# Kernel tuning notes

Hardware: AMD Instinct MI355X
Metric: run time of the kernel (lower is better)

The kernel has to match this reference:

```python
import jax, jax.numpy as jnp
import numpy as np


def setup_inputs() -> dict:
    key = jax.random.key(0)
    k1, k2 = jax.random.split(key)
    B, Lq, Lv, D = 16, 2048, 2048, 1024
    query = jax.random.normal(k1, (B, Lq, D), dtype=jnp.float32)
    value = jax.random.normal(k2, (B, Lv, D), dtype=jnp.float32)
    return {"query": query, "value": value}


def reference(query, value):
    # score[b,q,k] = sum_d query[b,q,d] * value[b,k,d]   (NO 1/sqrt(d) scaling,
    # matching the original torch module)
    score = jnp.einsum("bqd,bkd->bqk", query, value)
    attn = jax.nn.softmax(score, axis=-1)  # softmax over the value/key axis
    context = jnp.einsum("bqk,bkd->bqd", attn, value)
    return (context, attn)
```

## Files before the change

kernel.cpp:

```cpp
#include <hip/hip_runtime.h>

typedef __bf16 bf16_t;
typedef __attribute__((ext_vector_type(4))) __bf16 bf16x4;
typedef __attribute__((ext_vector_type(8))) __bf16 bf16x8;
typedef __attribute__((ext_vector_type(4))) float f32x4;

constexpr int BATCH = 16;
constexpr int LQ = 2048;
constexpr int LV = 2048;
constexpr int DIM = 1024;

constexpr int BM = 128, BN = 128, BK = 32;

typedef __attribute__((address_space(1))) const unsigned int g_u32;
typedef __attribute__((address_space(3))) unsigned int l_u32;
__device__ __forceinline__ void glds16(const void* g, void* l) {
    __builtin_amdgcn_global_load_lds((g_u32*)g, (l_u32*)l, 16, 0, 0);
}

__global__ __launch_bounds__(256)
void prep_kernel(const float4* __restrict__ src, bf16x4* __restrict__ hi,
                 bf16x4* __restrict__ lo, int n4) {
    int i = blockIdx.x * 256 + threadIdx.x;
    const int stride = gridDim.x * 256;
    for (; i < n4; i += stride) {
        const float4 x = src[i];
        const float xs[4] = {x.x, x.y, x.z, x.w};
        bf16x4 h, l;
#pragma unroll
        for (int e = 0; e < 4; ++e) {
            bf16_t hh = (bf16_t)xs[e];
            h[e] = hh;
            l[e] = (bf16_t)(xs[e] - (float)hh);
        }
        hi[i] = h;
        lo[i] = l;
    }
}

__global__ __launch_bounds__(256)
void vt_kernel(const float* __restrict__ V, bf16_t* __restrict__ VT) {
    __shared__ float tile[64][33];
    const int b  = blockIdx.z;
    const int k0 = blockIdx.x * 64;
    const int d0 = blockIdx.y * 32;
    const int tid = threadIdx.x;
    const float* Vb  = V  + (size_t)b * LV * DIM;
    bf16_t*      VTb = VT + (size_t)b * DIM * LV;

    const int r = tid >> 3;
    const int c = (tid & 7) * 4;
#pragma unroll
    for (int h = 0; h < 2; ++h) {
        const float4 x = *(const float4*)(Vb + (size_t)(k0 + r + h * 32) * DIM + d0 + c);
        tile[r + h * 32][c]     = x.x;
        tile[r + h * 32][c + 1] = x.y;
        tile[r + h * 32][c + 2] = x.z;
        tile[r + h * 32][c + 3] = x.w;
    }
    __syncthreads();
    const int dd = tid >> 3;
    const int kk = (tid & 7) * 8;
    bf16x8 o;
#pragma unroll
    for (int j = 0; j < 8; ++j) o[j] = (bf16_t)tile[kk + j][dd];
    *(bf16x8*)&VTb[(size_t)(d0 + dd) * LV + k0 + kk] = o;
}

__global__ __launch_bounds__(256, 3)
void gemm1_glds(const bf16_t* __restrict__ Qh, const bf16_t* __restrict__ Ql,
                const bf16_t* __restrict__ Vh, const bf16_t* __restrict__ Vl,
                float* __restrict__ S) {
    __shared__ __align__(16) bf16_t Ah[BM][BK];
    __shared__ __align__(16) bf16_t Al[BM][BK];
    __shared__ __align__(16) bf16_t Bh[BN][BK];
    __shared__ __align__(16) bf16_t Bl[BN][BK];

    const int b  = blockIdx.z;
    const int m0 = blockIdx.y * BM;
    const int n0 = blockIdx.x * BN;
    const bf16_t* Qhb = Qh + (size_t)b * LQ * DIM;
    const bf16_t* Qlb = Ql + (size_t)b * LQ * DIM;
    const bf16_t* Vhb = Vh + (size_t)b * LV * DIM;
    const bf16_t* Vlb = Vl + (size_t)b * LV * DIM;
    float*        Sb  = S  + (size_t)b * LQ * LV;

    const int tid  = threadIdx.x;
    const int lane = tid & 63;
    const int wave = tid >> 6;
    const int wm   = (wave >> 1) * 64;
    const int wn   = (wave & 1) * 64;
    const int l15  = lane & 15;
    const int quad = lane >> 4;

    const int srow = tid >> 2;
    const int sseg = (tid & 3) * 8;

    f32x4 acc[4][4];
#pragma unroll
    for (int i = 0; i < 4; ++i)
#pragma unroll
        for (int j = 0; j < 4; ++j) {
            f32x4 z = {0.f, 0.f, 0.f, 0.f};
            acc[i][j] = z;
        }

    for (int k0 = 0; k0 < DIM; k0 += BK) {
        glds16(Qhb + (size_t)(m0 + srow) * DIM + k0 + sseg,      &Ah[srow][sseg]);
        glds16(Qhb + (size_t)(m0 + srow + 64) * DIM + k0 + sseg, &Ah[srow + 64][sseg]);
        glds16(Qlb + (size_t)(m0 + srow) * DIM + k0 + sseg,      &Al[srow][sseg]);
        glds16(Qlb + (size_t)(m0 + srow + 64) * DIM + k0 + sseg, &Al[srow + 64][sseg]);
        glds16(Vhb + (size_t)(n0 + srow) * DIM + k0 + sseg,      &Bh[srow][sseg]);
        glds16(Vhb + (size_t)(n0 + srow + 64) * DIM + k0 + sseg, &Bh[srow + 64][sseg]);
        glds16(Vlb + (size_t)(n0 + srow) * DIM + k0 + sseg,      &Bl[srow][sseg]);
        glds16(Vlb + (size_t)(n0 + srow + 64) * DIM + k0 + sseg, &Bl[srow + 64][sseg]);
        __syncthreads();

        bf16x8 ah[4], al[4], bh[4], bl[4];
#pragma unroll
        for (int i = 0; i < 4; ++i) {
            ah[i] = *(const bf16x8*)&Ah[wm + i * 16 + l15][quad * 8];
            al[i] = *(const bf16x8*)&Al[wm + i * 16 + l15][quad * 8];
            bh[i] = *(const bf16x8*)&Bh[wn + i * 16 + l15][quad * 8];
            bl[i] = *(const bf16x8*)&Bl[wn + i * 16 + l15][quad * 8];
        }
#pragma unroll
        for (int i = 0; i < 4; ++i)
#pragma unroll
            for (int j = 0; j < 4; ++j) {
                acc[i][j] = __builtin_amdgcn_mfma_f32_16x16x32_bf16(ah[i], bh[j], acc[i][j], 0, 0, 0);
                acc[i][j] = __builtin_amdgcn_mfma_f32_16x16x32_bf16(ah[i], bl[j], acc[i][j], 0, 0, 0);
                acc[i][j] = __builtin_amdgcn_mfma_f32_16x16x32_bf16(al[i], bh[j], acc[i][j], 0, 0, 0);
            }
        __syncthreads();
    }

#pragma unroll
    for (int i = 0; i < 4; ++i)
#pragma unroll
        for (int j = 0; j < 4; ++j)
#pragma unroll
            for (int r = 0; r < 4; ++r) {
                const int row = m0 + wm + i * 16 + quad * 4 + r;
                const int col = n0 + wn + j * 16 + l15;
                Sb[(size_t)row * LV + col] = acc[i][j][r];
            }
}

__global__ __launch_bounds__(256)
void softmax_b16(float* __restrict__ S, bf16_t* __restrict__ S16) {
    __shared__ float red[8];
    const size_t row = blockIdx.x;
    float* p = S + row * (size_t)LV;
    bf16_t* p16 = S16 + row * (size_t)LV;
    const int tid  = threadIdx.x;
    const int lane = tid & 63;
    const int wave = tid >> 6;

    float4 v0 = ((const float4*)p)[tid];
    float4 v1 = ((const float4*)p)[tid + 256];

    float m = fmaxf(fmaxf(fmaxf(v0.x, v0.y), fmaxf(v0.z, v0.w)),
                    fmaxf(fmaxf(v1.x, v1.y), fmaxf(v1.z, v1.w)));
#pragma unroll
    for (int off = 32; off > 0; off >>= 1) m = fmaxf(m, __shfl_xor(m, off));
    if (lane == 0) red[wave] = m;
    __syncthreads();
    m = fmaxf(fmaxf(red[0], red[1]), fmaxf(red[2], red[3]));

    float e0 = __expf(v0.x - m), e1 = __expf(v0.y - m);
    float e2 = __expf(v0.z - m), e3 = __expf(v0.w - m);
    float e4 = __expf(v1.x - m), e5 = __expf(v1.y - m);
    float e6 = __expf(v1.z - m), e7 = __expf(v1.w - m);

    float s = ((e0 + e1) + (e2 + e3)) + ((e4 + e5) + (e6 + e7));
#pragma unroll
    for (int off = 32; off > 0; off >>= 1) s += __shfl_xor(s, off);
    if (lane == 0) red[4 + wave] = s;
    __syncthreads();
    s = (red[4] + red[5]) + (red[6] + red[7]);

    const float inv = 1.0f / s;
    v0.x = e0 * inv; v0.y = e1 * inv; v0.z = e2 * inv; v0.w = e3 * inv;
    v1.x = e4 * inv; v1.y = e5 * inv; v1.z = e6 * inv; v1.w = e7 * inv;
    ((float4*)p)[tid]       = v0;
    ((float4*)p)[tid + 256] = v1;

    bf16x4 h0, h1;
    h0[0] = (bf16_t)v0.x; h0[1] = (bf16_t)v0.y; h0[2] = (bf16_t)v0.z; h0[3] = (bf16_t)v0.w;
    h1[0] = (bf16_t)v1.x; h1[1] = (bf16_t)v1.y; h1[2] = (bf16_t)v1.z; h1[3] = (bf16_t)v1.w;
    ((bf16x4*)p16)[tid]       = h0;
    ((bf16x4*)p16)[tid + 256] = h1;
}

__global__ __launch_bounds__(256, 3)
void gemm2_glds(const bf16_t* __restrict__ P16, const bf16_t* __restrict__ VT,
                float* __restrict__ C) {
    __shared__ __align__(16) bf16_t As[BM][BK];
    __shared__ __align__(16) bf16_t Bs[BN][BK];

    const int b  = blockIdx.z;
    const int m0 = blockIdx.y * BM;
    const int n0 = blockIdx.x * BN;
    const bf16_t* Pb = P16 + (size_t)b * LQ * LV;
    const bf16_t* Vb = VT  + (size_t)b * DIM * LV;
    float*        Cb = C   + (size_t)b * LQ * DIM;

    const int tid  = threadIdx.x;
    const int lane = tid & 63;
    const int wave = tid >> 6;
    const int wm   = (wave >> 1) * 64;
    const int wn   = (wave & 1) * 64;
    const int l15  = lane & 15;
    const int quad = lane >> 4;

    const int srow = tid >> 2;
    const int sseg = (tid & 3) * 8;

    f32x4 acc[4][4];
#pragma unroll
    for (int i = 0; i < 4; ++i)
#pragma unroll
        for (int j = 0; j < 4; ++j) {
            f32x4 z = {0.f, 0.f, 0.f, 0.f};
            acc[i][j] = z;
        }

    for (int k0 = 0; k0 < LV; k0 += BK) {
        glds16(Pb + (size_t)(m0 + srow) * LV + k0 + sseg,      &As[srow][sseg]);
        glds16(Pb + (size_t)(m0 + srow + 64) * LV + k0 + sseg, &As[srow + 64][sseg]);
        glds16(Vb + (size_t)(n0 + srow) * LV + k0 + sseg,      &Bs[srow][sseg]);
        glds16(Vb + (size_t)(n0 + srow + 64) * LV + k0 + sseg, &Bs[srow + 64][sseg]);
        __syncthreads();

        bf16x8 af[4], bfr[4];
#pragma unroll
        for (int i = 0; i < 4; ++i) {
            af[i]  = *(const bf16x8*)&As[wm + i * 16 + l15][quad * 8];
            bfr[i] = *(const bf16x8*)&Bs[wn + i * 16 + l15][quad * 8];
        }
#pragma unroll
        for (int i = 0; i < 4; ++i)
#pragma unroll
            for (int j = 0; j < 4; ++j)
                acc[i][j] = __builtin_amdgcn_mfma_f32_16x16x32_bf16(af[i], bfr[j], acc[i][j], 0, 0, 0);
        __syncthreads();
    }

#pragma unroll
    for (int i = 0; i < 4; ++i)
#pragma unroll
        for (int j = 0; j < 4; ++j)
#pragma unroll
            for (int r = 0; r < 4; ++r) {
                const int row = m0 + wm + i * 16 + quad * 4 + r;
                const int col = n0 + wn + j * 16 + l15;
                Cb[(size_t)row * DIM + col] = acc[i][j][r];
            }
}

__global__ __launch_bounds__(256, 2)
void gemm1_fb(const float* __restrict__ Q, const float* __restrict__ V,
              float* __restrict__ S) {
    __shared__ __align__(16) bf16_t Ahi[BM][BK];
    __shared__ __align__(16) bf16_t Alo[BM][BK];
    __shared__ __align__(16) bf16_t Bhi[BN][BK];
    __shared__ __align__(16) bf16_t Blo[BN][BK];

    const int b  = blockIdx.z;
    const int m0 = blockIdx.y * BM;
    const int n0 = blockIdx.x * BN;
    const float* Qb = Q + (size_t)b * LQ * DIM;
    const float* Vb = V + (size_t)b * LV * DIM;
    float*       Sb = S + (size_t)b * LQ * LV;

    const int tid  = threadIdx.x;
    const int lane = tid & 63;
    const int wave = tid >> 6;
    const int wm   = (wave >> 1) * 64;
    const int wn   = (wave & 1) * 64;
    const int l15  = lane & 15;
    const int quad = lane >> 4;
    const int srow = tid >> 3;
    const int scol = (tid & 7) * 4;

    f32x4 acc[4][4];
#pragma unroll
    for (int i = 0; i < 4; ++i)
#pragma unroll
        for (int j = 0; j < 4; ++j) {
            f32x4 z = {0.f, 0.f, 0.f, 0.f};
            acc[i][j] = z;
        }

    for (int k0 = 0; k0 < DIM; k0 += BK) {
#pragma unroll
        for (int p = 0; p < 4; ++p) {
            const int r = p * 32 + srow;
            const float4 qa = *(const float4*)(Qb + (size_t)(m0 + r) * DIM + k0 + scol);
            const float4 va = *(const float4*)(Vb + (size_t)(n0 + r) * DIM + k0 + scol);
            const float qx[4] = {qa.x, qa.y, qa.z, qa.w};
            const float vx[4] = {va.x, va.y, va.z, va.w};
            bf16x4 qh, ql, vh, vl;
#pragma unroll
            for (int e = 0; e < 4; ++e) {
                bf16_t h = (bf16_t)qx[e];
                qh[e] = h; ql[e] = (bf16_t)(qx[e] - (float)h);
                bf16_t h2 = (bf16_t)vx[e];
                vh[e] = h2; vl[e] = (bf16_t)(vx[e] - (float)h2);
            }
            *(bf16x4*)&Ahi[r][scol] = qh;
            *(bf16x4*)&Alo[r][scol] = ql;
            *(bf16x4*)&Bhi[r][scol] = vh;
            *(bf16x4*)&Blo[r][scol] = vl;
        }
        __syncthreads();
        bf16x8 ah[4], al[4], bh[4], bl[4];
#pragma unroll
        for (int i = 0; i < 4; ++i) {
            ah[i] = *(const bf16x8*)&Ahi[wm + i * 16 + l15][quad * 8];
            al[i] = *(const bf16x8*)&Alo[wm + i * 16 + l15][quad * 8];
            bh[i] = *(const bf16x8*)&Bhi[wn + i * 16 + l15][quad * 8];
            bl[i] = *(const bf16x8*)&Blo[wn + i * 16 + l15][quad * 8];
        }
#pragma unroll
        for (int i = 0; i < 4; ++i)
#pragma unroll
            for (int j = 0; j < 4; ++j) {
                acc[i][j] = __builtin_amdgcn_mfma_f32_16x16x32_bf16(ah[i], bh[j], acc[i][j], 0, 0, 0);
                acc[i][j] = __builtin_amdgcn_mfma_f32_16x16x32_bf16(ah[i], bl[j], acc[i][j], 0, 0, 0);
                acc[i][j] = __builtin_amdgcn_mfma_f32_16x16x32_bf16(al[i], bh[j], acc[i][j], 0, 0, 0);
            }
        __syncthreads();
    }
#pragma unroll
    for (int i = 0; i < 4; ++i)
#pragma unroll
        for (int j = 0; j < 4; ++j)
#pragma unroll
            for (int r = 0; r < 4; ++r) {
                const int row = m0 + wm + i * 16 + quad * 4 + r;
                const int col = n0 + wn + j * 16 + l15;
                Sb[(size_t)row * LV + col] = acc[i][j][r];
            }
}

__global__ __launch_bounds__(256)
void softmax_fb(float* __restrict__ S) {
    __shared__ float red[8];
    const size_t row = blockIdx.x;
    float* p = S + row * (size_t)LV;
    const int tid  = threadIdx.x;
    const int lane = tid & 63;
    const int wave = tid >> 6;
    float4 v0 = ((const float4*)p)[tid];
    float4 v1 = ((const float4*)p)[tid + 256];
    float m = fmaxf(fmaxf(fmaxf(v0.x, v0.y), fmaxf(v0.z, v0.w)),
                    fmaxf(fmaxf(v1.x, v1.y), fmaxf(v1.z, v1.w)));
#pragma unroll
    for (int off = 32; off > 0; off >>= 1) m = fmaxf(m, __shfl_xor(m, off));
    if (lane == 0) red[wave] = m;
    __syncthreads();
    m = fmaxf(fmaxf(red[0], red[1]), fmaxf(red[2], red[3]));
    float e0 = __expf(v0.x - m), e1 = __expf(v0.y - m);
    float e2 = __expf(v0.z - m), e3 = __expf(v0.w - m);
    float e4 = __expf(v1.x - m), e5 = __expf(v1.y - m);
    float e6 = __expf(v1.z - m), e7 = __expf(v1.w - m);
    float s = ((e0 + e1) + (e2 + e3)) + ((e4 + e5) + (e6 + e7));
#pragma unroll
    for (int off = 32; off > 0; off >>= 1) s += __shfl_xor(s, off);
    if (lane == 0) red[4 + wave] = s;
    __syncthreads();
    s = (red[4] + red[5]) + (red[6] + red[7]);
    const float inv = 1.0f / s;
    v0.x = e0 * inv; v0.y = e1 * inv; v0.z = e2 * inv; v0.w = e3 * inv;
    v1.x = e4 * inv; v1.y = e5 * inv; v1.z = e6 * inv; v1.w = e7 * inv;
    ((float4*)p)[tid]       = v0;
    ((float4*)p)[tid + 256] = v1;
}

__global__ __launch_bounds__(256, 2)
void gemm2_fb(const float* __restrict__ P, const bf16_t* __restrict__ VT,
              float* __restrict__ C) {
    __shared__ __align__(16) bf16_t As[BM][BK];
    __shared__ __align__(16) bf16_t Bs[BN][BK];
    const int b  = blockIdx.z;
    const int m0 = blockIdx.y * BM;
    const int n0 = blockIdx.x * BN;
    const float*  Pb = P  + (size_t)b * LQ * LV;
    const bf16_t* Vb = VT + (size_t)b * DIM * LV;
    float*        Cb = C  + (size_t)b * LQ * DIM;
    const int tid  = threadIdx.x;
    const int lane = tid & 63;
    const int wave = tid >> 6;
    const int wm   = (wave >> 1) * 64;
    const int wn   = (wave & 1) * 64;
    const int l15  = lane & 15;
    const int quad = lane >> 4;
    const int arow = tid >> 3;
    const int acol = (tid & 7) * 4;
    const int brow = tid >> 2;
    const int bseg = (tid & 3) * 8;
    f32x4 acc[4][4];
#pragma unroll
    for (int i = 0; i < 4; ++i)
#pragma unroll
        for (int j = 0; j < 4; ++j) {
            f32x4 z = {0.f, 0.f, 0.f, 0.f};
            acc[i][j] = z;
        }
    for (int k0 = 0; k0 < LV; k0 += BK) {
#pragma unroll
        for (int p4 = 0; p4 < 4; ++p4) {
            const int r = p4 * 32 + arow;
            const float4 a = *(const float4*)(Pb + (size_t)(m0 + r) * LV + k0 + acol);
            bf16x4 hv;
            hv[0] = (bf16_t)a.x; hv[1] = (bf16_t)a.y;
            hv[2] = (bf16_t)a.z; hv[3] = (bf16_t)a.w;
            *(bf16x4*)&As[r][acol] = hv;
        }
#pragma unroll
        for (int p4 = 0; p4 < 2; ++p4) {
            const int r = p4 * 64 + brow;
            *(bf16x8*)&Bs[r][bseg] =
                *(const bf16x8*)(Vb + (size_t)(n0 + r) * LV + k0 + bseg);
        }
        __syncthreads();
        bf16x8 af[4], bfr[4];
#pragma unroll
        for (int i = 0; i < 4; ++i) {
            af[i]  = *(const bf16x8*)&As[wm + i * 16 + l15][quad * 8];
            bfr[i] = *(const bf16x8*)&Bs[wn + i * 16 + l15][quad * 8];
        }
#pragma unroll
        for (int i = 0; i < 4; ++i)
#pragma unroll
            for (int j = 0; j < 4; ++j)
                acc[i][j] = __builtin_amdgcn_mfma_f32_16x16x32_bf16(af[i], bfr[j], acc[i][j], 0, 0, 0);
        __syncthreads();
    }
#pragma unroll
    for (int i = 0; i < 4; ++i)
#pragma unroll
        for (int j = 0; j < 4; ++j)
#pragma unroll
            for (int r = 0; r < 4; ++r) {
                const int row = m0 + wm + i * 16 + quad * 4 + r;
                const int col = n0 + wn + j * 16 + l15;
                Cb[(size_t)row * DIM + col] = acc[i][j][r];
            }
}

extern "C" void kernel_launch(void* const* d_in, const int* in_sizes, int n_in,
                              void* d_out, int out_size, void* d_ws, size_t ws_size,
                              hipStream_t stream) {
    const float* Q = (const float*)d_in[0];
    const float* V = (const float*)d_in[1];
    float* ctx  = (float*)d_out;
    float* attn = ctx + (size_t)BATCH * LQ * DIM;
    char* ws = (char*)d_ws;

    const size_t EL = (size_t)BATCH * LQ * DIM;
    const size_t SZ = EL * sizeof(bf16_t);

    if (ws_size >= 5 * SZ) {
        bf16_t* Qh  = (bf16_t*)ws;
        bf16_t* Ql  = Qh + EL;
        bf16_t* Vh  = Ql + EL;
        bf16_t* Vl  = Vh + EL;
        bf16_t* VT  = (bf16_t*)(ws + 4 * SZ);
        bf16_t* P16 = (bf16_t*)ws;

        prep_kernel<<<4096, 256, 0, stream>>>((const float4*)Q, (bf16x4*)Qh, (bf16x4*)Ql, (int)(EL / 4));
        prep_kernel<<<4096, 256, 0, stream>>>((const float4*)V, (bf16x4*)Vh, (bf16x4*)Vl, (int)(EL / 4));
        vt_kernel<<<dim3(LV / 64, DIM / 32, BATCH), 256, 0, stream>>>(V, VT);
        gemm1_glds<<<dim3(LV / BN, LQ / BM, BATCH), 256, 0, stream>>>(Qh, Ql, Vh, Vl, attn);
        softmax_b16<<<BATCH * LQ, 256, 0, stream>>>(attn, P16);
        gemm2_glds<<<dim3(DIM / BN, LQ / BM, BATCH), 256, 0, stream>>>(P16, VT, ctx);
    } else if (ws_size >= 3 * SZ) {
        bf16_t* VT  = (bf16_t*)ws;
        bf16_t* P16 = (bf16_t*)(ws + SZ);
        vt_kernel<<<dim3(LV / 64, DIM / 32, BATCH), 256, 0, stream>>>(V, VT);
        gemm1_fb<<<dim3(LV / BN, LQ / BM, BATCH), 256, 0, stream>>>(Q, V, attn);
        softmax_b16<<<BATCH * LQ, 256, 0, stream>>>(attn, P16);
        gemm2_glds<<<dim3(DIM / BN, LQ / BM, BATCH), 256, 0, stream>>>(P16, VT, ctx);
    } else {
        bf16_t* VT = (bf16_t*)ws;
        vt_kernel<<<dim3(LV / 64, DIM / 32, BATCH), 256, 0, stream>>>(V, VT);
        gemm1_fb<<<dim3(LV / BN, LQ / BM, BATCH), 256, 0, stream>>>(Q, V, attn);
        softmax_fb<<<BATCH * LQ, 256, 0, stream>>>(attn);
        gemm2_fb<<<dim3(DIM / BN, LQ / BM, BATCH), 256, 0, stream>>>(attn, VT, ctx);
    }
}
```

Before: 1.264 ms.

## Rewrite score GEMM with 256x256 tiles, double-buffered LDS and swizzle

Replaces the first GEMM (split bf16 hi/lo, three MFMAs per product) with a 512-thread kernel that computes 256x256 output tiles. It double-buffers K-slices in 128KB of dynamic LDS via global_load_lds, swizzles the LDS layout to avoid bank conflicts, and interleaves fragment loads with MFMA quadrants under s_setprio. The aim is more data reuse per loaded byte and overlap of global loads with compute. In exchange it uses much more LDS and more registers per thread, which lowers occupancy, and relies on manual vmcnt waits and many barriers.

```diff
diff --git a/kernel.cpp b/kernel.cpp
--- a/kernel.cpp
+++ b/kernel.cpp
@@ -67,18 +67,16 @@
     *(bf16x8*)&VTb[(size_t)(d0 + dd) * LV + k0 + kk] = o;
 }
 
-__global__ __launch_bounds__(256, 3)
-void gemm1_glds(const bf16_t* __restrict__ Qh, const bf16_t* __restrict__ Ql,
-                const bf16_t* __restrict__ Vh, const bf16_t* __restrict__ Vl,
-                float* __restrict__ S) {
-    __shared__ __align__(16) bf16_t Ah[BM][BK];
-    __shared__ __align__(16) bf16_t Al[BM][BK];
-    __shared__ __align__(16) bf16_t Bh[BN][BK];
-    __shared__ __align__(16) bf16_t Bl[BN][BK];
+__global__ __launch_bounds__(512, 2)
+void gemm1_v2(const bf16_t* __restrict__ Qh, const bf16_t* __restrict__ Ql,
+              const bf16_t* __restrict__ Vh, const bf16_t* __restrict__ Vl,
+              float* __restrict__ S) {
+    extern __shared__ __align__(16) char smem[];
+    bf16_t* lds = (bf16_t*)smem;
 
     const int b  = blockIdx.z;
-    const int m0 = blockIdx.y * BM;
-    const int n0 = blockIdx.x * BN;
+    const int m0 = blockIdx.y * 256;
+    const int n0 = blockIdx.x * 256;
     const bf16_t* Qhb = Qh + (size_t)b * LQ * DIM;
     const bf16_t* Qlb = Ql + (size_t)b * LQ * DIM;
     const bf16_t* Vhb = Vh + (size_t)b * LV * DIM;
@@ -88,55 +86,112 @@
     const int tid  = threadIdx.x;
     const int lane = tid & 63;
     const int wave = tid >> 6;
-    const int wm   = (wave >> 1) * 64;
-    const int wn   = (wave & 1) * 64;
+    const int wm   = (wave >> 2) * 128;
+    const int wn   = (wave & 3) * 64;
     const int l15  = lane & 15;
     const int quad = lane >> 4;
+    const int swz  = (l15 >> 1) & 3;
+    const int rq   = (quad ^ swz) * 8;
 
     const int srow = tid >> 2;
-    const int sseg = (tid & 3) * 8;
-
-    f32x4 acc[4][4];
-#pragma unroll
-    for (int i = 0; i < 4; ++i)
+    const int sseg = (((tid & 3) ^ ((tid >> 3) & 3)) * 8);
+    const int sdst = tid * 8;
+
+#define STAGE8(BUF, K0) do {                                                        \
+    bf16_t* Lb = lds + (BUF) * 32768;                                               \
+    glds16(Qhb + (size_t)(m0 + srow      ) * DIM + (K0) + sseg, Lb +         sdst); \
+    glds16(Qhb + (size_t)(m0 + srow + 128) * DIM + (K0) + sseg, Lb +  4096 + sdst); \
+    glds16(Qlb + (size_t)(m0 + srow      ) * DIM + (K0) + sseg, Lb +  8192 + sdst); \
+    glds16(Qlb + (size_t)(m0 + srow + 128) * DIM + (K0) + sseg, Lb + 12288 + sdst); \
+    glds16(Vhb + (size_t)(n0 + srow      ) * DIM + (K0) + sseg, Lb + 16384 + sdst); \
+    glds16(Vhb + (size_t)(n0 + srow + 128) * DIM + (K0) + sseg, Lb + 20480 + sdst); \
+    glds16(Vlb + (size_t)(n0 + srow      ) * DIM + (K0) + sseg, Lb + 24576 + sdst); \
+    glds16(Vlb + (size_t)(n0 + srow + 128) * DIM + (K0) + sseg, Lb + 28672 + sdst); \
+} while (0)
+
+#define LOADA(QI) do {                                                       \
+    _Pragma("unroll")                                                        \
+    for (int ii = 0; ii < 4; ++ii) {                                         \
+        const int row = wm + ((QI) * 4 + ii) * 16 + l15;                     \
+        ah[ii] = *(const bf16x8*)(bufp +        row * 32 + rq);              \
+        al[ii] = *(const bf16x8*)(bufp + 8192 + row * 32 + rq);              \
+    }                                                                        \
+} while (0)
+
+#define LOADB(QJ) do {                                                       \
+    _Pragma("unroll")                                                        \
+    for (int jj = 0; jj < 2; ++jj) {                                         \
+        const int row = wn + ((QJ) * 2 + jj) * 16 + l15;                     \
+        bh[(QJ) * 2 + jj] = *(const bf16x8*)(bufp + 16384 + row * 32 + rq);  \
+        bl[(QJ) * 2 + jj] = *(const bf16x8*)(bufp + 24576 + row * 32 + rq);  \
+    }                                                                        \
+} while (0)
+
+#define MFMAQ(QI, QJ) do {                                                   \
+    _Pragma("unroll")                                                        \
+    for (int ii = 0; ii < 4; ++ii)                                           \
+    _Pragma("unroll")                                                        \
+    for (int jj = 0; jj < 2; ++jj)                                           \
+        acc[(QI)*4+ii][(QJ)*2+jj] = __builtin_amdgcn_mfma_f32_16x16x32_bf16( \
+            ah[ii], bh[(QJ)*2+jj], acc[(QI)*4+ii][(QJ)*2+jj], 0, 0, 0);      \
+    _Pragma("unroll")                                                        \
+    for (int ii = 0; ii < 4; ++ii)                                           \
+    _Pragma("unroll")                                                        \
+    for (int jj = 0; jj < 2; ++jj)                                           \
+        acc[(QI)*4+ii][(QJ)*2+jj] = __builtin_amdgcn_mfma_f32_16x16x32_bf16( \
+            ah[ii], bl[(QJ)*2+jj], acc[(QI)*4+ii][(QJ)*2+jj], 0, 0, 0);      \
+    _Pragma("unroll")                                                        \
+    for (int ii = 0; ii < 4; ++ii)                                           \
+    _Pragma("unroll")                                                        \
+    for (int jj = 0; jj < 2; ++jj)                                           \
+        acc[(QI)*4+ii][(QJ)*2+jj] = __builtin_amdgcn_mfma_f32_16x16x32_bf16( \
+            al[ii], bh[(QJ)*2+jj], acc[(QI)*4+ii][(QJ)*2+jj], 0, 0, 0);      \
+} while (0)
+
+    f32x4 acc[8][4];
+#pragma unroll
+    for (int i = 0; i < 8; ++i)
 #pragma unroll
         for (int j = 0; j < 4; ++j) {
             f32x4 z = {0.f, 0.f, 0.f, 0.f};
             acc[i][j] = z;
         }
 
-    for (int k0 = 0; k0 < DIM; k0 += BK) {
-        glds16(Qhb + (size_t)(m0 + srow) * DIM + k0 + sseg,      &Ah[srow][sseg]);
-        glds16(Qhb + (size_t)(m0 + srow + 64) * DIM + k0 + sseg, &Ah[srow + 64][sseg]);
-        glds16(Qlb + (size_t)(m0 + srow) * DIM + k0 + sseg,      &Al[srow][sseg]);
-        glds16(Qlb + (size_t)(m0 + srow + 64) * DIM + k0 + sseg, &Al[srow + 64][sseg]);
-        glds16(Vhb + (size_t)(n0 + srow) * DIM + k0 + sseg,      &Bh[srow][sseg]);
-        glds16(Vhb + (size_t)(n0 + srow + 64) * DIM + k0 + sseg, &Bh[srow + 64][sseg]);
-        glds16(Vlb + (size_t)(n0 + srow) * DIM + k0 + sseg,      &Bl[srow][sseg]);
-        glds16(Vlb + (size_t)(n0 + srow + 64) * DIM + k0 + sseg, &Bl[srow + 64][sseg]);
-        __syncthreads();
-
-        bf16x8 ah[4], al[4], bh[4], bl[4];
-#pragma unroll
-        for (int i = 0; i < 4; ++i) {
-            ah[i] = *(const bf16x8*)&Ah[wm + i * 16 + l15][quad * 8];
-            al[i] = *(const bf16x8*)&Al[wm + i * 16 + l15][quad * 8];
-            bh[i] = *(const bf16x8*)&Bh[wn + i * 16 + l15][quad * 8];
-            bl[i] = *(const bf16x8*)&Bl[wn + i * 16 + l15][quad * 8];
-        }
-#pragma unroll
-        for (int i = 0; i < 4; ++i)
-#pragma unroll
-            for (int j = 0; j < 4; ++j) {
-                acc[i][j] = __builtin_amdgcn_mfma_f32_16x16x32_bf16(ah[i], bh[j], acc[i][j], 0, 0, 0);
-                acc[i][j] = __builtin_amdgcn_mfma_f32_16x16x32_bf16(ah[i], bl[j], acc[i][j], 0, 0, 0);
-                acc[i][j] = __builtin_amdgcn_mfma_f32_16x16x32_bf16(al[i], bh[j], acc[i][j], 0, 0, 0);
-            }
-        __syncthreads();
-    }
-
-#pragma unroll
-    for (int i = 0; i < 4; ++i)
+    bf16x8 ah[4], al[4], bh[4], bl[4];
+
+    STAGE8(0, 0);
+
+    for (int t = 0; t < 32; ++t) {
+        const bf16_t* bufp = lds + (t & 1) * 32768;
+        if (t < 31) {
+            STAGE8((t & 1) ^ 1, (t + 1) * 32);
+            asm volatile("s_waitcnt vmcnt(8)" ::: "memory");
+        } else {
+            asm volatile("s_waitcnt vmcnt(0)" ::: "memory");
+        }
+        __builtin_amdgcn_s_barrier();
+
+        LOADA(0); LOADB(0);
+        __builtin_amdgcn_s_barrier();
+        __builtin_amdgcn_s_setprio(1); MFMAQ(0, 0); __builtin_amdgcn_s_setprio(0);
+        __builtin_amdgcn_s_barrier();
+
+        LOADB(1);
+        __builtin_amdgcn_s_barrier();
+        __builtin_amdgcn_s_setprio(1); MFMAQ(0, 1); __builtin_amdgcn_s_setprio(0);
+        __builtin_amdgcn_s_barrier();
+
+        LOADA(1);
+        __builtin_amdgcn_s_barrier();
+        __builtin_amdgcn_s_setprio(1); MFMAQ(1, 0); __builtin_amdgcn_s_setprio(0);
+        __builtin_amdgcn_s_barrier();
+
+        __builtin_amdgcn_s_setprio(1); MFMAQ(1, 1); __builtin_amdgcn_s_setprio(0);
+        __builtin_amdgcn_s_barrier();
+    }
+
+#pragma unroll
+    for (int i = 0; i < 8; ++i)
 #pragma unroll
         for (int j = 0; j < 4; ++j)
 #pragma unroll
@@ -145,6 +200,11 @@
                 const int col = n0 + wn + j * 16 + l15;
                 Sb[(size_t)row * LV + col] = acc[i][j][r];
             }
+
+#undef STAGE8
+#undef LOADA
+#undef LOADB
+#undef MFMAQ
 }
 
 __global__ __launch_bounds__(256)
@@ -464,6 +524,13 @@
     const size_t SZ = EL * sizeof(bf16_t);
 
     if (ws_size >= 5 * SZ) {
+        static bool attr_set = false;
+        if (!attr_set) {
+            (void)hipFuncSetAttribute((const void*)gemm1_v2,
+                                      hipFuncAttributeMaxDynamicSharedMemorySize,
+                                      131072);
+            attr_set = true;
+        }
         bf16_t* Qh  = (bf16_t*)ws;
         bf16_t* Ql  = Qh + EL;
         bf16_t* Vh  = Ql + EL;
@@ -474,7 +541,7 @@
         prep_kernel<<<4096, 256, 0, stream>>>((const float4*)Q, (bf16x4*)Qh, (bf16x4*)Ql, (int)(EL / 4));
         prep_kernel<<<4096, 256, 0, stream>>>((const float4*)V, (bf16x4*)Vh, (bf16x4*)Vl, (int)(EL / 4));
         vt_kernel<<<dim3(LV / 64, DIM / 32, BATCH), 256, 0, stream>>>(V, VT);
-        gemm1_glds<<<dim3(LV / BN, LQ / BM, BATCH), 256, 0, stream>>>(Qh, Ql, Vh, Vl, attn);
+        gemm1_v2<<<dim3(LV / 256, LQ / 256, BATCH), 512, 131072, stream>>>(Qh, Ql, Vh, Vl, attn);
         softmax_b16<<<BATCH * LQ, 256, 0, stream>>>(attn, P16);
         gemm2_glds<<<dim3(DIM / BN, LQ / BM, BATCH), 256, 0, stream>>>(P16, VT, ctx);
     } else if (ws_size >= 3 * SZ) {
```

Result: no change. 1.266 ms (+0.2%).
